# Performance work log

Hardware: AMD Instinct MI355X
Metric: run time of the kernel (lower is better)

Reference implementation:

```python
import jax, jax.numpy as jnp
import numpy as np

OUT = 7   # output_size
SR = 2    # sampling_ratio


def _roi_align(feat_bhwc, rois, batch_idx, sx, sy):
    """RoIAlign (torchvision semantics, aligned=False) with per-axis spatial scale.
    feat_bhwc: [B,H,W,C]; rois: [K,4] (x1,y1,x2,y2) in padded-image coords;
    batch_idx: [K] int32; returns [K,C,OUT,OUT]."""
    B, H, W, C = feat_bhwc.shape
    K = rois.shape[0]
    x1 = rois[:, 0] * sx
    y1 = rois[:, 1] * sy
    x2 = rois[:, 2] * sx
    y2 = rois[:, 3] * sy
    bw = jnp.maximum(x2 - x1, 1.0) / OUT   # bin width  [K]
    bh = jnp.maximum(y2 - y1, 1.0) / OUT   # bin height [K]
    # sample position j in [0, OUT*SR): offset (j+0.5)/SR bins from roi start
    g = (jnp.arange(OUT * SR, dtype=feat_bhwc.dtype) + 0.5) / SR
    ys = y1[:, None] + g[None, :] * bh[:, None]   # [K, P] with P = OUT*SR
    xs = x1[:, None] + g[None, :] * bw[:, None]   # [K, P]
    Y = ys[:, :, None]                            # [K,P,1]
    X = xs[:, None, :]                            # [K,1,P]
    valid = (Y >= -1.0) & (Y <= H) & (X >= -1.0) & (X <= W)  # [K,P,P]
    Yc = jnp.clip(Y, 0.0, H - 1)
    Xc = jnp.clip(X, 0.0, W - 1)
    y0f = jnp.floor(Yc)
    x0f = jnp.floor(Xc)
    ly = Yc - y0f
    lx = Xc - x0f
    hy = 1.0 - ly
    hx = 1.0 - lx
    y0i = y0f.astype(jnp.int32)
    x0i = x0f.astype(jnp.int32)
    y1i = jnp.minimum(y0i + 1, H - 1)
    x1i = jnp.minimum(x0i + 1, W - 1)
    b = batch_idx[:, None, None]                  # [K,1,1]

    def gat(yi, xi):
        # broadcasts indices to [K,P,P]; gathers [K,P,P,C]
        return feat_bhwc[b, yi, xi]

    out = ((hy * hx)[..., None] * gat(y0i, x0i)
           + (hy * lx)[..., None] * gat(y0i, x1i)
           + (ly * hx)[..., None] * gat(y1i, x0i)
           + (ly * lx)[..., None] * gat(y1i, x1i))
    out = out * valid[..., None].astype(out.dtype)
    # average SRxSR samples per output bin
    out = out.reshape(K, OUT, SR, OUT, SR, C).mean(axis=(2, 4))
    return out.transpose(0, 3, 1, 2)  # [K,C,OUT,OUT]


def reference(x0, x1, x2, boxes, ratio, offset, shape):
    B, C0, H0, W0 = x0.shape
    # bilinear upsample (half-pixel centers == torch align_corners=False) and concat
    up1 = jax.image.resize(x1, (B, x1.shape[1], H0, W0), method='bilinear')
    up2 = jax.image.resize(x2, (B, x2.shape[1], H0, W0), method='bilinear')
    feat = jnp.concatenate([x0, up1, up2], axis=1)      # [B, 3*C, H0, W0]
    feat_bhwc = feat.transpose(0, 2, 3, 1)
    # map boxes from original-image coords to padded/resized coords
    rH, rW = ratio[:, 0], ratio[:, 1]
    top, left = offset[:, 0], offset[:, 1]
    mul = jnp.stack([rW, rH, rW, rH], axis=-1)[:, None, :]   # [B,1,4]
    add = jnp.stack([left, top, left, top], axis=-1)[:, None, :]
    rois = (boxes * mul + add).reshape(-1, 4)                # [K,4]
    N = boxes.shape[1]
    batch_idx = jnp.repeat(jnp.arange(B, dtype=jnp.int32), N)
    # per-axis spatial scale from the first meta (as in the torch code)
    padded_h = jnp.floor(shape[0, 0] * rH[0] + 2.0 * top[0])
    padded_w = jnp.floor(shape[0, 1] * rW[0] + 2.0 * left[0])
    sx = W0 / padded_w
    sy = H0 / padded_h
    return _roi_align(feat_bhwc, rois, batch_idx, sx, sy)   # [B*N, 3*C, 7, 7]


def setup_inputs():
    key = jax.random.key(0)
    k = jax.random.split(key, 5)
    B, C, N = 2, 256, 128
    IH, IW = 800.0, 1216.0  # original image size; stride-8 top level -> 100x152
    x0 = jax.random.normal(k[0], (B, C, 100, 152), jnp.float32)
    x1 = jax.random.normal(k[1], (B, C, 50, 76), jnp.float32)
    x2 = jax.random.normal(k[2], (B, C, 25, 38), jnp.float32)
    xy = jax.random.uniform(k[3], (B, N, 2)) * jnp.array([IW - 64.0, IH - 64.0], jnp.float32)
    wh = 16.0 + jax.random.uniform(k[4], (B, N, 2)) * 200.0
    boxes = jnp.concatenate([xy, jnp.minimum(xy + wh, jnp.array([IW, IH], jnp.float32))], axis=-1)
    ratio = jnp.ones((B, 2), jnp.float32)
    offset = jnp.zeros((B, 2), jnp.float32)
    shape = jnp.tile(jnp.array([[IH, IW]], jnp.float32), (B, 1))
    return dict(x0=x0, x1=x1, x2=x2, boxes=boxes, ratio=ratio, offset=offset, shape=shape)
```

## Files before the change

kernel.cpp:

```cpp
#include <hip/hip_runtime.h>
#include <hip/hip_bf16.h>

constexpr int B  = 2;
constexpr int C  = 256;
constexpr int H0 = 100, W0 = 152;
constexpr int H1 = 50,  W1 = 76;
constexpr int H2 = 25,  W2 = 38;
constexpr int N  = 128;
constexpr int K  = B * N;
constexpr int CT = 3 * C;
constexpr int OUTS = 7;

#define DEV __device__ __forceinline__

template <typename T> DEV float ldf(const T* p) { return *p; }
template <> DEV float ldf<__hip_bfloat16>(const __hip_bfloat16* p) { return __bfloat162float(*p); }
template <typename T> DEV void stf(T* p, float v) { *p = v; }
template <> DEV void stf<__hip_bfloat16>(__hip_bfloat16* p, float v) { *p = __float2bfloat16(v); }

template <typename T> DEV void st4(T* p, float a, float b, float c, float d);
template <> DEV void st4<float>(float* p, float a, float b, float c, float d) {
  *reinterpret_cast<float4*>(p) = make_float4(a, b, c, d);
}
template <> DEV void st4<__hip_bfloat16>(__hip_bfloat16* p, float a, float b, float c, float d) {
  union { __hip_bfloat16 h[4]; uint2 u; } pk;
  pk.h[0] = __float2bfloat16(a); pk.h[1] = __float2bfloat16(b);
  pk.h[2] = __float2bfloat16(c); pk.h[3] = __float2bfloat16(d);
  *reinterpret_cast<uint2*>(p) = pk.u;
}

template <typename T>
__global__ __launch_bounds__(256) void fuse_kernel(
    const float* __restrict__ x0, const float* __restrict__ x1,
    const float* __restrict__ x2, T* __restrict__ feat) {
  __shared__ float lds[64][153];
  const int blk  = blockIdx.x;
  const int tile = blk % 12;
  const int by   = blk / 12;
  const int y    = by % H0;
  const int b    = by / H0;
  const int t    = threadIdx.x;
  const int level = tile >> 2;
  const int c0l   = (tile & 3) * 64;

  if (level == 0) {
    for (int i = 0; i < 38; ++i) {
      const int lin = i * 256 + t;
      const int cl = lin / 152, x = lin % 152;
      lds[cl][x] = x0[(((size_t)b * C + (c0l + cl)) * H0 + y) * W0 + x];
    }
  } else if (level == 1) {
    float fy = fminf(fmaxf(y * 0.5f - 0.25f, 0.f), (float)(H1 - 1));
    int   y0i = (int)floorf(fy);
    float ly  = fy - (float)y0i;
    int   y1i = min(y0i + 1, H1 - 1);
    for (int i = 0; i < 38; ++i) {
      const int lin = i * 256 + t;
      const int cl = lin / 152, x = lin % 152;
      float fx = fminf(fmaxf(x * 0.5f - 0.25f, 0.f), (float)(W1 - 1));
      int   x0i = (int)floorf(fx);
      float lx  = fx - (float)x0i;
      int   x1i = min(x0i + 1, W1 - 1);
      const float* base = x1 + ((size_t)b * C + (c0l + cl)) * (H1 * W1);
      float a = base[y0i * W1 + x0i], bb = base[y0i * W1 + x1i];
      float c = base[y1i * W1 + x0i], d  = base[y1i * W1 + x1i];
      lds[cl][x] = (1.f - ly) * (a + lx * (bb - a)) + ly * (c + lx * (d - c));
    }
  } else {
    float fy = fminf(fmaxf((y + 0.5f) * 0.25f - 0.5f, 0.f), (float)(H2 - 1));
    int   y0i = (int)floorf(fy);
    float ly  = fy - (float)y0i;
    int   y1i = min(y0i + 1, H2 - 1);
    for (int i = 0; i < 38; ++i) {
      const int lin = i * 256 + t;
      const int cl = lin / 152, x = lin % 152;
      float fx = fminf(fmaxf((x + 0.5f) * 0.25f - 0.5f, 0.f), (float)(W2 - 1));
      int   x0i = (int)floorf(fx);
      float lx  = fx - (float)x0i;
      int   x1i = min(x0i + 1, W2 - 1);
      const float* base = x2 + ((size_t)b * C + (c0l + cl)) * (H2 * W2);
      float a = base[y0i * W2 + x0i], bb = base[y0i * W2 + x1i];
      float c = base[y1i * W2 + x0i], d  = base[y1i * W2 + x1i];
      lds[cl][x] = (1.f - ly) * (a + lx * (bb - a)) + ly * (c + lx * (d - c));
    }
  }
  __syncthreads();
  const int cg = tile * 64;
  for (int i = 0; i < 10; ++i) {
    const int lin = i * 256 + t;
    if (lin < 152 * 16) {
      const int x = lin >> 4, cq = lin & 15;
      T* p = feat + (((size_t)b * H0 + y) * W0 + x) * CT + cg + cq * 4;
      st4(p, lds[cq * 4 + 0][x], lds[cq * 4 + 1][x],
             lds[cq * 4 + 2][x], lds[cq * 4 + 3][x]);
    }
  }
}

template <typename T>
__global__ __launch_bounds__(256) void roi_kernel(
    const T* __restrict__ feat, const float* __restrict__ boxes,
    const float* __restrict__ ratio, const float* __restrict__ offset,
    const float* __restrict__ shape, float* __restrict__ out) {
  __shared__ float lds[256 * 49];
  const int blk = blockIdx.x;
  const int cg  = blk % 3;
  const int k   = blk / 3;
  const int b   = k >> 7;
  const int t   = threadIdx.x;
  const int c   = cg * 256 + t;

  const float padded_h = floorf(shape[0] * ratio[0] + 2.f * offset[0]);
  const float padded_w = floorf(shape[1] * ratio[1] + 2.f * offset[1]);
  const float sx = (float)W0 / padded_w;
  const float sy = (float)H0 / padded_h;
  const float rHb = ratio[b * 2 + 0], rWb = ratio[b * 2 + 1];
  const float topb = offset[b * 2 + 0], leftb = offset[b * 2 + 1];
  const float* bx = boxes + (size_t)k * 4;
  const float x1s = (bx[0] * rWb + leftb) * sx;
  const float y1s = (bx[1] * rHb + topb) * sy;
  const float x2s = (bx[2] * rWb + leftb) * sx;
  const float y2s = (bx[3] * rHb + topb) * sy;
  const float bw = fmaxf(x2s - x1s, 1.f) / OUTS;
  const float bh = fmaxf(y2s - y1s, 1.f) / OUTS;

  float hx[14], lx[14];
  int xo0[14], xo1[14];
  #pragma unroll
  for (int s = 0; s < 14; ++s) {
    const float X = x1s + ((float)s * 0.5f + 0.25f) * bw;
    const bool vx = (X >= -1.f) && (X <= (float)W0);
    const float Xc = fminf(fmaxf(X, 0.f), (float)(W0 - 1));
    const float xf = floorf(Xc);
    const float l  = Xc - xf;
    const int x0i = (int)xf;
    const int x1i = min(x0i + 1, W0 - 1);
    hx[s]  = vx ? (1.f - l) : 0.f;
    lx[s]  = vx ? l : 0.f;
    xo0[s] = x0i * CT;
    xo1[s] = x1i * CT;
  }

  const T* fb = feat + (size_t)b * (H0 * W0 * CT) + c;

  for (int ph = 0; ph < OUTS; ++ph) {
    float acc[OUTS] = {0.f, 0.f, 0.f, 0.f, 0.f, 0.f, 0.f};
    #pragma unroll
    for (int iy = 0; iy < 2; ++iy) {
      const float Y = y1s + ((float)ph + (float)iy * 0.5f + 0.25f) * bh;
      const bool vy = (Y >= -1.f) && (Y <= (float)H0);
      const float Yc = fminf(fmaxf(Y, 0.f), (float)(H0 - 1));
      const float yf = floorf(Yc);
      const float ly = Yc - yf;
      const int y0i = (int)yf;
      const int y1i = min(y0i + 1, H0 - 1);
      const float w0 = vy ? (1.f - ly) * 0.25f : 0.f;
      const float w1 = vy ? ly * 0.25f : 0.f;
      const T* r0 = fb + (size_t)y0i * (W0 * CT);
      const T* r1 = fb + (size_t)y1i * (W0 * CT);
      #pragma unroll
      for (int pw = 0; pw < OUTS; ++pw) {
        #pragma unroll
        for (int ix = 0; ix < 2; ++ix) {
          const int s = pw * 2 + ix;
          const float a00 = ldf(r0 + xo0[s]);
          const float a01 = ldf(r0 + xo1[s]);
          const float a10 = ldf(r1 + xo0[s]);
          const float a11 = ldf(r1 + xo1[s]);
          acc[pw] += w0 * (hx[s] * a00 + lx[s] * a01) +
                     w1 * (hx[s] * a10 + lx[s] * a11);
        }
      }
    }
    #pragma unroll
    for (int pw = 0; pw < OUTS; ++pw) lds[t * 49 + ph * 7 + pw] = acc[pw];
  }
  __syncthreads();
  float* ob = out + (size_t)k * (CT * 49) + (size_t)cg * (256 * 49);
  const float4* ls = reinterpret_cast<const float4*>(lds);
  float4* os = reinterpret_cast<float4*>(ob);
  for (int i = 0; i < 13; ++i) {
    const int idx = i * 256 + t;
    if (idx < 3136) os[idx] = ls[idx];
  }
}

extern "C" void kernel_launch(void* const* d_in, const int* in_sizes, int n_in,
                              void* d_out, int out_size, void* d_ws, size_t ws_size,
                              hipStream_t stream) {
  const float* x0     = (const float*)d_in[0];
  const float* x1     = (const float*)d_in[1];
  const float* x2     = (const float*)d_in[2];
  const float* boxes  = (const float*)d_in[3];
  const float* ratio  = (const float*)d_in[4];
  const float* offset = (const float*)d_in[5];
  const float* shape  = (const float*)d_in[6];
  float* out = (float*)d_out;

  const size_t feat_elems = (size_t)B * H0 * W0 * CT;
  const dim3 g1(B * H0 * 12), blk(256);
  const dim3 g2(K * 3);

  if (ws_size >= feat_elems * sizeof(float)) {
    float* feat = (float*)d_ws;
    fuse_kernel<float><<<g1, blk, 0, stream>>>(x0, x1, x2, feat);
    roi_kernel<float><<<g2, blk, 0, stream>>>(feat, boxes, ratio, offset, shape, out);
  } else {
    __hip_bfloat16* feat = (__hip_bfloat16*)d_ws;
    fuse_kernel<__hip_bfloat16><<<g1, blk, 0, stream>>>(x0, x1, x2, feat);
    roi_kernel<__hip_bfloat16><<<g2, blk, 0, stream>>>(feat, boxes, ratio, offset, shape, out);
  }
}
```

Baseline: 167.5 us.

## Always store fused feature map in bf16 and vectorize separable upsample loads

Drops the fp32 workspace path so the concatenated feature map is always written and read in bf16, halving intermediate traffic for both kernels. The fuse kernel now loads source rows with float4/float2 vector reads, and it does the bilinear upsample separably: vertical interpolation goes into LDS and horizontal interpolation happens on readout. Scaled coordinates are folded into constants and floorf is replaced by a truncating int cast, which is safe because the values are clamped non-negative. The cost is reduced feature precision (bf16 rounding) in the RoI gather.

New measurement: 139.3 us. 1.2x faster.

```diff
diff --git a/kernel.cpp b/kernel.cpp
--- a/kernel.cpp
+++ b/kernel.cpp
@@ -13,27 +13,19 @@
 
 #define DEV __device__ __forceinline__
 
-template <typename T> DEV float ldf(const T* p) { return *p; }
-template <> DEV float ldf<__hip_bfloat16>(const __hip_bfloat16* p) { return __bfloat162float(*p); }
-template <typename T> DEV void stf(T* p, float v) { *p = v; }
-template <> DEV void stf<__hip_bfloat16>(__hip_bfloat16* p, float v) { *p = __float2bfloat16(v); }
-
-template <typename T> DEV void st4(T* p, float a, float b, float c, float d);
-template <> DEV void st4<float>(float* p, float a, float b, float c, float d) {
-  *reinterpret_cast<float4*>(p) = make_float4(a, b, c, d);
-}
-template <> DEV void st4<__hip_bfloat16>(__hip_bfloat16* p, float a, float b, float c, float d) {
+DEV float ldbf(const __hip_bfloat16* p) { return __bfloat162float(*p); }
+
+DEV void st4bf(__hip_bfloat16* p, float a, float b, float c, float d) {
   union { __hip_bfloat16 h[4]; uint2 u; } pk;
   pk.h[0] = __float2bfloat16(a); pk.h[1] = __float2bfloat16(b);
   pk.h[2] = __float2bfloat16(c); pk.h[3] = __float2bfloat16(d);
   *reinterpret_cast<uint2*>(p) = pk.u;
 }
 
-template <typename T>
 __global__ __launch_bounds__(256) void fuse_kernel(
     const float* __restrict__ x0, const float* __restrict__ x1,
-    const float* __restrict__ x2, T* __restrict__ feat) {
-  __shared__ float lds[64][153];
+    const float* __restrict__ x2, __hip_bfloat16* __restrict__ feat) {
+  __shared__ float buf[64 * 153];
   const int blk  = blockIdx.x;
   const int tile = blk % 12;
   const int by   = blk / 12;
@@ -43,63 +35,114 @@
   const int level = tile >> 2;
   const int c0l   = (tile & 3) * 64;
 
+  __hip_bfloat16* const orow =
+      feat + (((size_t)b * H0 + y) * W0) * CT + tile * 64;
+
   if (level == 0) {
-    for (int i = 0; i < 38; ++i) {
-      const int lin = i * 256 + t;
-      const int cl = lin / 152, x = lin % 152;
-      lds[cl][x] = x0[(((size_t)b * C + (c0l + cl)) * H0 + y) * W0 + x];
+    const float* src = x0 + (((size_t)b * C + c0l) * H0 + y) * W0;
+    for (int i = 0; i < 10; ++i) {
+      const int lin = i * 256 + t;
+      if (lin < 2432) {
+        const int cl = lin / 38, xq = lin % 38;
+        const float4 v =
+            *reinterpret_cast<const float4*>(src + (size_t)cl * (H0 * W0) + xq * 4);
+        float* d = &buf[cl * 153 + xq * 4];
+        d[0] = v.x; d[1] = v.y; d[2] = v.z; d[3] = v.w;
+      }
+    }
+    __syncthreads();
+    for (int i = 0; i < 10; ++i) {
+      const int lin = i * 256 + t;
+      if (lin < 2432) {
+        const int x = lin >> 4, cq = lin & 15;
+        st4bf(orow + (size_t)x * CT + cq * 4,
+              buf[(cq * 4 + 0) * 153 + x], buf[(cq * 4 + 1) * 153 + x],
+              buf[(cq * 4 + 2) * 153 + x], buf[(cq * 4 + 3) * 153 + x]);
+      }
     }
   } else if (level == 1) {
-    float fy = fminf(fmaxf(y * 0.5f - 0.25f, 0.f), (float)(H1 - 1));
-    int   y0i = (int)floorf(fy);
-    float ly  = fy - (float)y0i;
-    int   y1i = min(y0i + 1, H1 - 1);
-    for (int i = 0; i < 38; ++i) {
-      const int lin = i * 256 + t;
-      const int cl = lin / 152, x = lin % 152;
-      float fx = fminf(fmaxf(x * 0.5f - 0.25f, 0.f), (float)(W1 - 1));
-      int   x0i = (int)floorf(fx);
-      float lx  = fx - (float)x0i;
-      int   x1i = min(x0i + 1, W1 - 1);
-      const float* base = x1 + ((size_t)b * C + (c0l + cl)) * (H1 * W1);
-      float a = base[y0i * W1 + x0i], bb = base[y0i * W1 + x1i];
-      float c = base[y1i * W1 + x0i], d  = base[y1i * W1 + x1i];
-      lds[cl][x] = (1.f - ly) * (a + lx * (bb - a)) + ly * (c + lx * (d - c));
+    const float fy = fminf(fmaxf(y * 0.5f - 0.25f, 0.f), (float)(H1 - 1));
+    const int   y0i = (int)fy;
+    const float ly  = fy - (float)y0i;
+    const int   y1i = min(y0i + 1, H1 - 1);
+    const int rstep = (y1i - y0i) * W1;
+    const float* s0 = x1 + (((size_t)b * C + c0l) * H1 + y0i) * W1;
+    for (int i = 0; i < 5; ++i) {
+      const int lin = i * 256 + t;
+      if (lin < 1216) {
+        const int cl = lin / 19, xq = lin % 19;
+        const float* p = s0 + (size_t)cl * (H1 * W1) + xq * 4;
+        const float4 v0 = *reinterpret_cast<const float4*>(p);
+        const float4 v1 = *reinterpret_cast<const float4*>(p + rstep);
+        float* d = &buf[cl * 81 + xq * 4];
+        d[0] = v0.x + ly * (v1.x - v0.x);
+        d[1] = v0.y + ly * (v1.y - v0.y);
+        d[2] = v0.z + ly * (v1.z - v0.z);
+        d[3] = v0.w + ly * (v1.w - v0.w);
+      }
+    }
+    __syncthreads();
+    for (int i = 0; i < 10; ++i) {
+      const int lin = i * 256 + t;
+      if (lin < 2432) {
+        const int x = lin >> 4, cq = lin & 15;
+        const float fx = fminf(fmaxf(x * 0.5f - 0.25f, 0.f), (float)(W1 - 1));
+        const int   x0i = (int)fx;
+        const float lx  = fx - (float)x0i;
+        const int   x1i = min(x0i + 1, W1 - 1);
+        const float* r = &buf[cq * 4 * 81];
+        float v[4];
+        #pragma unroll
+        for (int j = 0; j < 4; ++j) {
+          const float a = r[j * 81 + x0i], bb = r[j * 81 + x1i];
+          v[j] = a + lx * (bb - a);
+        }
+        st4bf(orow + (size_t)x * CT + cq * 4, v[0], v[1], v[2], v[3]);
+      }
     }
   } else {
-    float fy = fminf(fmaxf((y + 0.5f) * 0.25f - 0.5f, 0.f), (float)(H2 - 1));
-    int   y0i = (int)floorf(fy);
-    float ly  = fy - (float)y0i;
-    int   y1i = min(y0i + 1, H2 - 1);
-    for (int i = 0; i < 38; ++i) {
-      const int lin = i * 256 + t;
-      const int cl = lin / 152, x = lin % 152;
-      float fx = fminf(fmaxf((x + 0.5f) * 0.25f - 0.5f, 0.f), (float)(W2 - 1));
-      int   x0i = (int)floorf(fx);
-      float lx  = fx - (float)x0i;
-      int   x1i = min(x0i + 1, W2 - 1);
-      const float* base = x2 + ((size_t)b * C + (c0l + cl)) * (H2 * W2);
-      float a = base[y0i * W2 + x0i], bb = base[y0i * W2 + x1i];
-      float c = base[y1i * W2 + x0i], d  = base[y1i * W2 + x1i];
-      lds[cl][x] = (1.f - ly) * (a + lx * (bb - a)) + ly * (c + lx * (d - c));
-    }
-  }
-  __syncthreads();
-  const int cg = tile * 64;
-  for (int i = 0; i < 10; ++i) {
-    const int lin = i * 256 + t;
-    if (lin < 152 * 16) {
-      const int x = lin >> 4, cq = lin & 15;
-      T* p = feat + (((size_t)b * H0 + y) * W0 + x) * CT + cg + cq * 4;
-      st4(p, lds[cq * 4 + 0][x], lds[cq * 4 + 1][x],
-             lds[cq * 4 + 2][x], lds[cq * 4 + 3][x]);
-    }
-  }
-}
-
-template <typename T>
+    const float fy = fminf(fmaxf(y * 0.25f - 0.375f, 0.f), (float)(H2 - 1));
+    const int   y0i = (int)fy;
+    const float ly  = fy - (float)y0i;
+    const int   y1i = min(y0i + 1, H2 - 1);
+    const int rstep = (y1i - y0i) * W2;
+    const float* s0 = x2 + (((size_t)b * C + c0l) * H2 + y0i) * W2;
+    for (int i = 0; i < 5; ++i) {
+      const int lin = i * 256 + t;
+      if (lin < 1216) {
+        const int cl = lin / 19, xq = lin % 19;
+        const float* p = s0 + (size_t)cl * (H2 * W2) + xq * 2;
+        const float2 v0 = *reinterpret_cast<const float2*>(p);
+        const float2 v1 = *reinterpret_cast<const float2*>(p + rstep);
+        float* d = &buf[cl * 39 + xq * 2];
+        d[0] = v0.x + ly * (v1.x - v0.x);
+        d[1] = v0.y + ly * (v1.y - v0.y);
+      }
+    }
+    __syncthreads();
+    for (int i = 0; i < 10; ++i) {
+      const int lin = i * 256 + t;
+      if (lin < 2432) {
+        const int x = lin >> 4, cq = lin & 15;
+        const float fx = fminf(fmaxf(x * 0.25f - 0.375f, 0.f), (float)(W2 - 1));
+        const int   x0i = (int)fx;
+        const float lx  = fx - (float)x0i;
+        const int   x1i = min(x0i + 1, W2 - 1);
+        const float* r = &buf[cq * 4 * 39];
+        float v[4];
+        #pragma unroll
+        for (int j = 0; j < 4; ++j) {
+          const float a = r[j * 39 + x0i], bb = r[j * 39 + x1i];
+          v[j] = a + lx * (bb - a);
+        }
+        st4bf(orow + (size_t)x * CT + cq * 4, v[0], v[1], v[2], v[3]);
+      }
+    }
+  }
+}
+
 __global__ __launch_bounds__(256) void roi_kernel(
-    const T* __restrict__ feat, const float* __restrict__ boxes,
+    const __hip_bfloat16* __restrict__ feat, const float* __restrict__ boxes,
     const float* __restrict__ ratio, const float* __restrict__ offset,
     const float* __restrict__ shape, float* __restrict__ out) {
   __shared__ float lds[256 * 49];
@@ -141,7 +184,7 @@
     xo1[s] = x1i * CT;
   }
 
-  const T* fb = feat + (size_t)b * (H0 * W0 * CT) + c;
+  const __hip_bfloat16* fb = feat + (size_t)b * (H0 * W0 * CT) + c;
 
   for (int ph = 0; ph < OUTS; ++ph) {
     float acc[OUTS] = {0.f, 0.f, 0.f, 0.f, 0.f, 0.f, 0.f};
@@ -156,17 +199,17 @@
       const int y1i = min(y0i + 1, H0 - 1);
       const float w0 = vy ? (1.f - ly) * 0.25f : 0.f;
       const float w1 = vy ? ly * 0.25f : 0.f;
-      const T* r0 = fb + (size_t)y0i * (W0 * CT);
-      const T* r1 = fb + (size_t)y1i * (W0 * CT);
+      const __hip_bfloat16* r0 = fb + (size_t)y0i * (W0 * CT);
+      const __hip_bfloat16* r1 = fb + (size_t)y1i * (W0 * CT);
       #pragma unroll
       for (int pw = 0; pw < OUTS; ++pw) {
         #pragma unroll
         for (int ix = 0; ix < 2; ++ix) {
           const int s = pw * 2 + ix;
-          const float a00 = ldf(r0 + xo0[s]);
-          const float a01 = ldf(r0 + xo1[s]);
-          const float a10 = ldf(r1 + xo0[s]);
-          const float a11 = ldf(r1 + xo1[s]);
+          const float a00 = ldbf(r0 + xo0[s]);
+          const float a01 = ldbf(r0 + xo1[s]);
+          const float a10 = ldbf(r1 + xo0[s]);
+          const float a11 = ldbf(r1 + xo1[s]);
           acc[pw] += w0 * (hx[s] * a00 + lx[s] * a01) +
                      w1 * (hx[s] * a10 + lx[s] * a11);
         }
@@ -197,17 +240,11 @@
   const float* shape  = (const float*)d_in[6];
   float* out = (float*)d_out;
 
-  const size_t feat_elems = (size_t)B * H0 * W0 * CT;
-  const dim3 g1(B * H0 * 12), blk(256);
+  __hip_bfloat16* feat = (__hip_bfloat16*)d_ws;
+  const dim3 blk(256);
+  const dim3 g1(B * H0 * 12);
   const dim3 g2(K * 3);
 
-  if (ws_size >= feat_elems * sizeof(float)) {
-    float* feat = (float*)d_ws;
-    fuse_kernel<float><<<g1, blk, 0, stream>>>(x0, x1, x2, feat);
-    roi_kernel<float><<<g2, blk, 0, stream>>>(feat, boxes, ratio, offset, shape, out);
-  } else {
-    __hip_bfloat16* feat = (__hip_bfloat16*)d_ws;
-    fuse_kernel<__hip_bfloat16><<<g1, blk, 0, stream>>>(x0, x1, x2, feat);
-    roi_kernel<__hip_bfloat16><<<g2, blk, 0, stream>>>(feat, boxes, ratio, offset, shape, out);
-  }
-}
+  fuse_kernel<<<g1, blk, 0, stream>>>(x0, x1, x2, feat);
+  roi_kernel<<<g2, blk, 0, stream>>>(feat, boxes, ratio, offset, shape, out);
+}
```
